# Kernel optimization log

Hardware: AMD Instinct MI355X
Metric: run time of the kernel (lower is better)

## Reference

```python
import jax, jax.numpy as jnp
import numpy as np

TOP_K = 2  # MoEBlock default


def setup_inputs() -> dict:
    key = jax.random.key(0)
    ks = jax.random.split(key, 7)
    B_, S, D, F, E, R = 2, 2048, 1024, 4096, 4, 4
    x  = jax.random.normal(ks[0], (B_, S, D), dtype=jnp.float32)
    Wg = jax.random.normal(ks[1], (E, D), dtype=jnp.float32) * (1.0 / np.sqrt(D))
    bg = jnp.zeros((E,), dtype=jnp.float32)
    Wi = jax.random.normal(ks[2], (F, D), dtype=jnp.float32) * (1.0 / np.sqrt(D))
    Wo = jax.random.normal(ks[3], (D, F), dtype=jnp.float32) * (1.0 / np.sqrt(F))
    A  = jax.random.normal(ks[4], (E, R, D), dtype=jnp.float32) * (1.0 / np.sqrt(D))
    Bm = jax.random.normal(ks[5], (E, F, R), dtype=jnp.float32) * 0.01
    return {"x": x, "Wg": Wg, "bg": bg, "Wi": Wi, "Wo": Wo, "A": A, "B": Bm}


def reference(x, Wg, bg, Wi, Wo, A, B):
    E = Wg.shape[0]
    # ---- Router: softmax gate + top-k ----
    logits = jnp.einsum('bsd,ed->bse', x, Wg) + bg          # [B,S,E]
    scores = jax.nn.softmax(logits, axis=-1)
    topv, topi = jax.lax.top_k(scores, TOP_K)               # [B,S,K]
    # per-token combine weight for each expert (sum of matching top-k probs)
    w = jnp.sum(jax.nn.one_hot(topi, E, dtype=x.dtype) * topv[..., None], axis=-2)  # [B,S,E]
    # ---- Experts: shared frozen FFN + per-expert LoRA (dense, then masked) ----
    base = jnp.einsum('bsd,fd->bsf', x, Wi)                 # shared wi(x), [B,S,F]
    lora_low = jnp.einsum('bsd,erd->bser', x, A)            # [B,S,E,R]
    lora = jnp.einsum('bser,efr->bsef', lora_low, B)        # [B,S,E,F]
    h = jax.nn.relu(base[:, :, None, :] + lora)             # act(wi(x)+lora), [B,S,E,F]
    expert_out = jnp.einsum('bsef,df->bsed', h, Wo)         # wo(.), [B,S,E,D]
    # ---- Combine ----
    out = jnp.einsum('bse,bsed->bsd', w, expert_out)        # [B,S,D]
    return out
```

## Files before the change

kernel.cpp:

```cpp
#include <hip/hip_runtime.h>
#include <stdint.h>

#define BSz 4096
#define Ddim 1024
#define Fdim 4096
#define Edim 4
#define Rdim 4

typedef __attribute__((ext_vector_type(8))) short bf16x8;
typedef __attribute__((ext_vector_type(4))) float f32x4;

__device__ __forceinline__ unsigned short f2bf(float f) {
  union { float f; uint32_t u; } c; c.f = f;
  return (unsigned short)((c.u + 0x7fffu + ((c.u >> 16) & 1u)) >> 16);
}

__global__ __launch_bounds__(256) void cvt2_kernel(const float* __restrict__ wi,
                                                   const float* __restrict__ wo,
                                                   unsigned short* __restrict__ wib,
                                                   unsigned short* __restrict__ wob,
                                                   int n4) {
  int i = blockIdx.x * 256 + threadIdx.x;
  if (i >= n4) return;
  const float* src = (blockIdx.y == 0) ? wi : wo;
  unsigned short* dst = (blockIdx.y == 0) ? wib : wob;
  float4 v = ((const float4*)src)[i];
  ushort4 o;
  o.x = f2bf(v.x); o.y = f2bf(v.y); o.z = f2bf(v.z); o.w = f2bf(v.w);
  ((ushort4*)dst)[i] = o;
}

__global__ __launch_bounds__(256) void router_cvtx(const float* __restrict__ x,
                                                   const float* __restrict__ Wg,
                                                   const float* __restrict__ bg,
                                                   const float* __restrict__ Aw,
                                                   unsigned short* __restrict__ xb,
                                                   float* __restrict__ meta) {
  __shared__ float xs[Ddim];
  __shared__ float dots[Edim + Edim * Rdim];
  const int t = blockIdx.x;
  const float4* xt = (const float4*)(x + (size_t)t * Ddim);
  {
    const int i = threadIdx.x;
    float4 v = xt[i];
    ((float4*)xs)[i] = v;
    ushort4 o;
    o.x = f2bf(v.x); o.y = f2bf(v.y); o.z = f2bf(v.z); o.w = f2bf(v.w);
    ((ushort4*)(xb + (size_t)t * Ddim))[i] = o;
  }
  __syncthreads();
  const int wave = threadIdx.x >> 6, lane = threadIdx.x & 63;
  for (int d = wave * 5; d < wave * 5 + 5; ++d) {
    const float* wrow = (d < Edim) ? (Wg + (size_t)d * Ddim)
                                   : (Aw + (size_t)(d - Edim) * Ddim);
    float s = 0.f;
    for (int i = lane; i < Ddim; i += 64) s += xs[i] * wrow[i];
    for (int off = 32; off; off >>= 1) s += __shfl_down(s, off);
    if (lane == 0) dots[d] = s;
  }
  __syncthreads();
  if (threadIdx.x == 0) {
    float p[Edim];
    float m = -1e30f;
    for (int e = 0; e < Edim; ++e) { p[e] = dots[e] + bg[e]; m = fmaxf(m, p[e]); }
    float sum = 0.f;
    for (int e = 0; e < Edim; ++e) { p[e] = expf(p[e] - m); sum += p[e]; }
    const float inv = 1.f / sum;
    for (int e = 0; e < Edim; ++e) p[e] *= inv;
    int e0 = 0;
    for (int e = 1; e < Edim; ++e) if (p[e] > p[e0]) e0 = e;
    int e1 = (e0 == 0) ? 1 : 0;
    for (int e = 0; e < Edim; ++e) if (e != e0 && p[e] > p[e1]) e1 = e;
    float* mt = meta + (size_t)t * 16;
    mt[0] = (float)e0; mt[1] = (float)e1; mt[2] = p[e0]; mt[3] = p[e1];
    for (int r = 0; r < Rdim; ++r) {
      mt[4 + r] = dots[Edim + e0 * Rdim + r];
      mt[8 + r] = dots[Edim + e1 * Rdim + r];
    }
    mt[12] = 0.f; mt[13] = 0.f; mt[14] = 0.f; mt[15] = 0.f;
  }
}

template <int EPI>
__global__ __launch_bounds__(256, 4)
void gemm97(const unsigned short* __restrict__ Ag,
            const unsigned short* __restrict__ Bg,
            int K, int kslice, int Ncols,
            const float* __restrict__ meta,
            const float* __restrict__ B2,
            unsigned short* __restrict__ outg,
            float* __restrict__ outf,
            float* __restrict__ zbuf) {
  constexpr int BK = 64;
  __shared__ __align__(16) unsigned short sA[128 * BK];
  __shared__ __align__(16) unsigned short sB[128 * BK];

  const int tid = threadIdx.x;
  const int lane = tid & 63;
  const int wave = tid >> 6;
  const int wr = wave >> 1, wc = wave & 1;
  const int l16 = lane & 15, lhi = lane >> 4;

  const int nwg = gridDim.x * gridDim.y;
  const int lin = blockIdx.y * gridDim.x + blockIdx.x;
  const int cpx = nwg >> 3;
  const int swz = (lin & 7) * cpx + (lin >> 3);
  const int bx = swz % gridDim.x, by = swz / gridDim.x;
  const int bm = by * 128, bn = bx * 128;
  const int kbase = blockIdx.z * kslice;
  const int NT = kslice / BK;

  if (EPI == 0) {
    const float4 z4 = make_float4(0.f, 0.f, 0.f, 0.f);
#pragma unroll
    for (int zz = 0; zz < 4; ++zz)
      ((float4*)zbuf)[(size_t)lin * 1024 + zz * 256 + tid] = z4;
  }

  f32x4 acc[4][4] = {};

  const int srow = tid >> 3;
  const int scol = ((tid & 7) ^ (srow & 7)) * 8;
  const int ldst = tid * 8;
  const int xr = l16 & 7;

  for (int kt = 0; kt < NT; ++kt) {
    const int kof = kbase + kt * BK;
#pragma unroll
    for (int rr = 0; rr < 4; ++rr)
      __builtin_amdgcn_global_load_lds(
          (const __attribute__((address_space(1))) void*)(Ag + (size_t)(bm + srow + rr * 32) * K + kof + scol),
          (__attribute__((address_space(3))) void*)(sA + ldst + rr * 2048), 16, 0, 0);
#pragma unroll
    for (int rr = 0; rr < 4; ++rr)
      __builtin_amdgcn_global_load_lds(
          (const __attribute__((address_space(1))) void*)(Bg + (size_t)(bn + srow + rr * 32) * K + kof + scol),
          (__attribute__((address_space(3))) void*)(sB + ldst + rr * 2048), 16, 0, 0);
    __syncthreads();
#pragma unroll
    for (int kk = 0; kk < 2; ++kk) {
      bf16x8 af[4], bfv[4];
#pragma unroll
      for (int i = 0; i < 4; ++i) {
        af[i] = *(const bf16x8*)(sA + (wr * 64 + i * 16 + l16) * BK + (((kk * 4 + lhi) ^ xr) * 8));
        bfv[i] = *(const bf16x8*)(sB + (wc * 64 + i * 16 + l16) * BK + (((kk * 4 + lhi) ^ xr) * 8));
      }
#pragma unroll
      for (int i = 0; i < 4; ++i)
#pragma unroll
        for (int j = 0; j < 4; ++j)
          acc[i][j] = __builtin_amdgcn_mfma_f32_16x16x32_bf16(af[i], bfv[j], acc[i][j], 0, 0, 0);
    }
    __syncthreads();
  }

  if (EPI == 0) {
#pragma unroll
    for (int mi = 0; mi < 4; ++mi) {
#pragma unroll
      for (int r = 0; r < 4; ++r) {
        const int rowl = wr * 64 + mi * 16 + lhi * 4 + r;
        const int row = bm + rowl;
        const float* mt = meta + (size_t)row * 16;
        const int e0 = (int)mt[0], e1 = (int)mt[1];
        const float w0 = mt[2], w1 = mt[3];
        const float4 l0 = *(const float4*)(mt + 4);
        const float4 l1 = *(const float4*)(mt + 8);
        unsigned short* trow = (rowl < 64 ? sA + rowl * 128 : sB + (rowl - 64) * 128);
#pragma unroll
        for (int ni = 0; ni < 4; ++ni) {
          const int coll = wc * 64 + ni * 16 + l16;
          const int f = bn + coll;
          const float4 b0 = *(const float4*)(B2 + ((size_t)e0 * Fdim + f) * Rdim);
          const float4 b1 = *(const float4*)(B2 + ((size_t)e1 * Fdim + f) * Rdim);
          const float a = acc[mi][ni][r];
          const float lora0 = l0.x * b0.x + l0.y * b0.y + l0.z * b0.z + l0.w * b0.w;
          const float lora1 = l1.x * b1.x + l1.y * b1.y + l1.z * b1.z + l1.w * b1.w;
          const float gv = w0 * fmaxf(a + lora0, 0.f) + w1 * fmaxf(a + lora1, 0.f);
          trow[coll] = f2bf(gv);
        }
      }
    }
    __syncthreads();
#pragma unroll
    for (int rnd = 0; rnd < 8; ++rnd) {
      const int idx = rnd * 256 + tid;
      const int rowl = idx >> 4;
      const int chk = idx & 15;
      const unsigned short* src = (rowl < 64 ? sA + rowl * 128 : sB + (rowl - 64) * 128) + chk * 8;
      *(bf16x8*)(outg + (size_t)(bm + rowl) * Fdim + bn + chk * 8) = *(const bf16x8*)src;
    }
  } else {
#pragma unroll
    for (int mi = 0; mi < 4; ++mi)
#pragma unroll
      for (int ni = 0; ni < 4; ++ni)
#pragma unroll
        for (int r = 0; r < 4; ++r) {
          const int row = bm + wr * 64 + mi * 16 + lhi * 4 + r;
          const int col = bn + wc * 64 + ni * 16 + l16;
          unsafeAtomicAdd(&outf[(size_t)row * Ncols + col], acc[mi][ni][r]);
        }
  }
}

extern "C" void kernel_launch(void* const* d_in, const int* in_sizes, int n_in,
                              void* d_out, int out_size, void* d_ws, size_t ws_size,
                              hipStream_t stream) {
  const float* x  = (const float*)d_in[0];
  const float* Wg = (const float*)d_in[1];
  const float* bg = (const float*)d_in[2];
  const float* Wi = (const float*)d_in[3];
  const float* Wo = (const float*)d_in[4];
  const float* Aw = (const float*)d_in[5];
  const float* B2 = (const float*)d_in[6];
  float* out = (float*)d_out;

  unsigned short* xb  = (unsigned short*)d_ws;
  unsigned short* wib = xb  + (size_t)BSz  * Ddim;
  unsigned short* wob = wib + (size_t)Fdim * Ddim;
  unsigned short* g   = wob + (size_t)Ddim * Fdim;
  float* meta = (float*)(g + (size_t)BSz * Fdim);

  const int n4 = Fdim * Ddim / 4;
  cvt2_kernel<<<dim3((n4 + 255) / 256, 2), 256, 0, stream>>>(
      Wi, Wo, wib, wob, n4);

  router_cvtx<<<BSz, 256, 0, stream>>>(x, Wg, bg, Aw, xb, meta);

  gemm97<0><<<dim3(Fdim / 128, BSz / 128, 1), 256, 0, stream>>>(
      xb, wib, Ddim, Ddim, Fdim, meta, B2, g, nullptr, out);

  gemm97<1><<<dim3(Ddim / 128, BSz / 128, 2), 256, 0, stream>>>(
      g, wob, Fdim, Fdim / 2, Ddim, nullptr, nullptr, nullptr, out, nullptr);
}
```

Measured before the change: 168.5 us.

## Fuse weight conversion into router kernel and enlarge first GEMM tile to 256x128

Merges the bf16 conversion of Wi/Wo into the router/x-conversion kernel as extra blocks, removing a separate launch and letting both run concurrently. The first GEMM gets a dedicated kernel with 512 threads and a 256x128 tile, increasing operand reuse per block and halving the grid in M. Its epilogue stages the output in two halves through shared memory. The larger block lowers per-CU occupancy and adds more sync steps in the epilogue.

```diff
diff --git a/kernel.cpp b/kernel.cpp
--- a/kernel.cpp
+++ b/kernel.cpp
@@ -15,34 +15,35 @@
   return (unsigned short)((c.u + 0x7fffu + ((c.u >> 16) & 1u)) >> 16);
 }
 
-__global__ __launch_bounds__(256) void cvt2_kernel(const float* __restrict__ wi,
-                                                   const float* __restrict__ wo,
-                                                   unsigned short* __restrict__ wib,
-                                                   unsigned short* __restrict__ wob,
-                                                   int n4) {
-  int i = blockIdx.x * 256 + threadIdx.x;
-  if (i >= n4) return;
-  const float* src = (blockIdx.y == 0) ? wi : wo;
-  unsigned short* dst = (blockIdx.y == 0) ? wib : wob;
-  float4 v = ((const float4*)src)[i];
-  ushort4 o;
-  o.x = f2bf(v.x); o.y = f2bf(v.y); o.z = f2bf(v.z); o.w = f2bf(v.w);
-  ((ushort4*)dst)[i] = o;
-}
-
-__global__ __launch_bounds__(256) void router_cvtx(const float* __restrict__ x,
+__global__ __launch_bounds__(256) void prep_kernel(const float* __restrict__ x,
                                                    const float* __restrict__ Wg,
                                                    const float* __restrict__ bg,
                                                    const float* __restrict__ Aw,
+                                                   const float* __restrict__ Wi,
+                                                   const float* __restrict__ Wo,
                                                    unsigned short* __restrict__ xb,
+                                                   unsigned short* __restrict__ wib,
+                                                   unsigned short* __restrict__ wob,
                                                    float* __restrict__ meta) {
+  const int b = blockIdx.x;
+  if (b >= BSz) {
+    const int n4 = Fdim * Ddim / 4;
+    int i = (b - BSz) * 256 + threadIdx.x;
+    const float* src = (i < n4) ? Wi : Wo;
+    unsigned short* dst = (i < n4) ? wib : wob;
+    if (i >= n4) i -= n4;
+    float4 v = ((const float4*)src)[i];
+    ushort4 o;
+    o.x = f2bf(v.x); o.y = f2bf(v.y); o.z = f2bf(v.z); o.w = f2bf(v.w);
+    ((ushort4*)dst)[i] = o;
+    return;
+  }
   __shared__ float xs[Ddim];
   __shared__ float dots[Edim + Edim * Rdim];
-  const int t = blockIdx.x;
-  const float4* xt = (const float4*)(x + (size_t)t * Ddim);
+  const int t = b;
   {
     const int i = threadIdx.x;
-    float4 v = xt[i];
+    float4 v = ((const float4*)(x + (size_t)t * Ddim))[i];
     ((float4*)xs)[i] = v;
     ushort4 o;
     o.x = f2bf(v.x); o.y = f2bf(v.y); o.z = f2bf(v.z); o.w = f2bf(v.w);
@@ -81,16 +82,121 @@
   }
 }
 
-template <int EPI>
+__global__ __launch_bounds__(512, 2)
+void gemm1_w(const unsigned short* __restrict__ Ag,
+             const unsigned short* __restrict__ Bg,
+             const float* __restrict__ meta,
+             const float* __restrict__ B2,
+             unsigned short* __restrict__ outg,
+             float* __restrict__ zbuf) {
+  constexpr int K = Ddim, BK = 64;
+  __shared__ __align__(16) unsigned short sA[256 * BK];
+  __shared__ __align__(16) unsigned short sB[128 * BK];
+
+  const int tid = threadIdx.x;
+  const int lane = tid & 63;
+  const int wave = tid >> 6;
+  const int wr = wave >> 1, wc = wave & 1;
+  const int l16 = lane & 15, lhi = lane >> 4;
+
+  const int nwg = gridDim.x * gridDim.y;
+  const int lin = blockIdx.y * gridDim.x + blockIdx.x;
+  const int cpx = nwg >> 3;
+  const int swz = (lin & 7) * cpx + (lin >> 3);
+  const int bx = swz % gridDim.x, by = swz / gridDim.x;
+  const int bm = by * 256, bn = bx * 128;
+
+  {
+    const float4 z4 = make_float4(0.f, 0.f, 0.f, 0.f);
+#pragma unroll
+    for (int zz = 0; zz < 4; ++zz)
+      ((float4*)zbuf)[(size_t)lin * 2048 + zz * 512 + tid] = z4;
+  }
+
+  f32x4 acc[4][4] = {};
+
+  const int srow = tid >> 3;
+  const int scol = ((tid & 7) ^ (srow & 7)) * 8;
+  const int ldst = tid * 8;
+  const int xr = l16 & 7;
+
+  for (int kt = 0; kt < K / BK; ++kt) {
+    const int kof = kt * BK;
+#pragma unroll
+    for (int rr = 0; rr < 4; ++rr)
+      __builtin_amdgcn_global_load_lds(
+          (const __attribute__((address_space(1))) void*)(Ag + (size_t)(bm + srow + rr * 64) * K + kof + scol),
+          (__attribute__((address_space(3))) void*)(sA + ldst + rr * 4096), 16, 0, 0);
+#pragma unroll
+    for (int rr = 0; rr < 2; ++rr)
+      __builtin_amdgcn_global_load_lds(
+          (const __attribute__((address_space(1))) void*)(Bg + (size_t)(bn + srow + rr * 64) * K + kof + scol),
+          (__attribute__((address_space(3))) void*)(sB + ldst + rr * 4096), 16, 0, 0);
+    __syncthreads();
+#pragma unroll
+    for (int kk = 0; kk < 2; ++kk) {
+      bf16x8 af[4], bfv[4];
+#pragma unroll
+      for (int i = 0; i < 4; ++i) {
+        af[i] = *(const bf16x8*)(sA + (wr * 64 + i * 16 + l16) * BK + (((kk * 4 + lhi) ^ xr) * 8));
+        bfv[i] = *(const bf16x8*)(sB + (wc * 64 + i * 16 + l16) * BK + (((kk * 4 + lhi) ^ xr) * 8));
+      }
+#pragma unroll
+      for (int i = 0; i < 4; ++i)
+#pragma unroll
+        for (int j = 0; j < 4; ++j)
+          acc[i][j] = __builtin_amdgcn_mfma_f32_16x16x32_bf16(af[i], bfv[j], acc[i][j], 0, 0, 0);
+    }
+    __syncthreads();
+  }
+
+#pragma unroll
+  for (int half = 0; half < 2; ++half) {
+    if ((wr >> 1) == half) {
+#pragma unroll
+      for (int mi = 0; mi < 4; ++mi) {
+#pragma unroll
+        for (int r = 0; r < 4; ++r) {
+          const int rowl = wr * 64 + mi * 16 + lhi * 4 + r;
+          const int row = bm + rowl;
+          const float* mt = meta + (size_t)row * 16;
+          const int e0 = (int)mt[0], e1 = (int)mt[1];
+          const float w0 = mt[2], w1 = mt[3];
+          const float4 l0 = *(const float4*)(mt + 4);
+          const float4 l1 = *(const float4*)(mt + 8);
+#pragma unroll
+          for (int ni = 0; ni < 4; ++ni) {
+            const int coll = wc * 64 + ni * 16 + l16;
+            const int f = bn + coll;
+            const float4 b0 = *(const float4*)(B2 + ((size_t)e0 * Fdim + f) * Rdim);
+            const float4 b1 = *(const float4*)(B2 + ((size_t)e1 * Fdim + f) * Rdim);
+            const float a = acc[mi][ni][r];
+            const float lora0 = l0.x * b0.x + l0.y * b0.y + l0.z * b0.z + l0.w * b0.w;
+            const float lora1 = l1.x * b1.x + l1.y * b1.y + l1.z * b1.z + l1.w * b1.w;
+            const float gv = w0 * fmaxf(a + lora0, 0.f) + w1 * fmaxf(a + lora1, 0.f);
+            sA[(rowl - half * 128) * 128 + coll] = f2bf(gv);
+          }
+        }
+      }
+    }
+    __syncthreads();
+#pragma unroll
+    for (int rnd = 0; rnd < 4; ++rnd) {
+      const int idx = rnd * 512 + tid;
+      const int rowl2 = idx >> 4;
+      const int chk = idx & 15;
+      *(bf16x8*)(outg + (size_t)(bm + half * 128 + rowl2) * Fdim + bn + chk * 8) =
+          *(const bf16x8*)(sA + rowl2 * 128 + chk * 8);
+    }
+    __syncthreads();
+  }
+}
+
 __global__ __launch_bounds__(256, 4)
-void gemm97(const unsigned short* __restrict__ Ag,
-            const unsigned short* __restrict__ Bg,
-            int K, int kslice, int Ncols,
-            const float* __restrict__ meta,
-            const float* __restrict__ B2,
-            unsigned short* __restrict__ outg,
-            float* __restrict__ outf,
-            float* __restrict__ zbuf) {
+void gemm2_w(const unsigned short* __restrict__ Ag,
+             const unsigned short* __restrict__ Bg,
+             int K, int kslice, int Ncols,
+             float* __restrict__ outf) {
   constexpr int BK = 64;
   __shared__ __align__(16) unsigned short sA[128 * BK];
   __shared__ __align__(16) unsigned short sB[128 * BK];
@@ -110,13 +216,6 @@
   const int kbase = blockIdx.z * kslice;
   const int NT = kslice / BK;
 
-  if (EPI == 0) {
-    const float4 z4 = make_float4(0.f, 0.f, 0.f, 0.f);
-#pragma unroll
-    for (int zz = 0; zz < 4; ++zz)
-      ((float4*)zbuf)[(size_t)lin * 1024 + zz * 256 + tid] = z4;
-  }
-
   f32x4 acc[4][4] = {};
 
   const int srow = tid >> 3;
@@ -154,54 +253,16 @@
     __syncthreads();
   }
 
-  if (EPI == 0) {
-#pragma unroll
-    for (int mi = 0; mi < 4; ++mi) {
+#pragma unroll
+  for (int mi = 0; mi < 4; ++mi)
+#pragma unroll
+    for (int ni = 0; ni < 4; ++ni)
 #pragma unroll
       for (int r = 0; r < 4; ++r) {
-        const int rowl = wr * 64 + mi * 16 + lhi * 4 + r;
-        const int row = bm + rowl;
-        const float* mt = meta + (size_t)row * 16;
-        const int e0 = (int)mt[0], e1 = (int)mt[1];
-        const float w0 = mt[2], w1 = mt[3];
-        const float4 l0 = *(const float4*)(mt + 4);
-        const float4 l1 = *(const float4*)(mt + 8);
-        unsigned short* trow = (rowl < 64 ? sA + rowl * 128 : sB + (rowl - 64) * 128);
-#pragma unroll
-        for (int ni = 0; ni < 4; ++ni) {
-          const int coll = wc * 64 + ni * 16 + l16;
-          const int f = bn + coll;
-          const float4 b0 = *(const float4*)(B2 + ((size_t)e0 * Fdim + f) * Rdim);
-          const float4 b1 = *(const float4*)(B2 + ((size_t)e1 * Fdim + f) * Rdim);
-          const float a = acc[mi][ni][r];
-          const float lora0 = l0.x * b0.x + l0.y * b0.y + l0.z * b0.z + l0.w * b0.w;
-          const float lora1 = l1.x * b1.x + l1.y * b1.y + l1.z * b1.z + l1.w * b1.w;
-          const float gv = w0 * fmaxf(a + lora0, 0.f) + w1 * fmaxf(a + lora1, 0.f);
-          trow[coll] = f2bf(gv);
-        }
-      }
-    }
-    __syncthreads();
-#pragma unroll
-    for (int rnd = 0; rnd < 8; ++rnd) {
-      const int idx = rnd * 256 + tid;
-      const int rowl = idx >> 4;
-      const int chk = idx & 15;
-      const unsigned short* src = (rowl < 64 ? sA + rowl * 128 : sB + (rowl - 64) * 128) + chk * 8;
-      *(bf16x8*)(outg + (size_t)(bm + rowl) * Fdim + bn + chk * 8) = *(const bf16x8*)src;
-    }
-  } else {
-#pragma unroll
-    for (int mi = 0; mi < 4; ++mi)
-#pragma unroll
-      for (int ni = 0; ni < 4; ++ni)
-#pragma unroll
-        for (int r = 0; r < 4; ++r) {
-          const int row = bm + wr * 64 + mi * 16 + lhi * 4 + r;
-          const int col = bn + wc * 64 + ni * 16 + l16;
-          unsafeAtomicAdd(&outf[(size_t)row * Ncols + col], acc[mi][ni][r]);
-        }
-  }
+        const int row = bm + wr * 64 + mi * 16 + lhi * 4 + r;
+        const int col = bn + wc * 64 + ni * 16 + l16;
+        unsafeAtomicAdd(&outf[(size_t)row * Ncols + col], acc[mi][ni][r]);
+      }
 }
 
 extern "C" void kernel_launch(void* const* d_in, const int* in_sizes, int n_in,
@@ -222,15 +283,12 @@
   unsigned short* g   = wob + (size_t)Ddim * Fdim;
   float* meta = (float*)(g + (size_t)BSz * Fdim);
 
-  const int n4 = Fdim * Ddim / 4;
-  cvt2_kernel<<<dim3((n4 + 255) / 256, 2), 256, 0, stream>>>(
-      Wi, Wo, wib, wob, n4);
-
-  router_cvtx<<<BSz, 256, 0, stream>>>(x, Wg, bg, Aw, xb, meta);
-
-  gemm97<0><<<dim3(Fdim / 128, BSz / 128, 1), 256, 0, stream>>>(
-      xb, wib, Ddim, Ddim, Fdim, meta, B2, g, nullptr, out);
-
-  gemm97<1><<<dim3(Ddim / 128, BSz / 128, 2), 256, 0, stream>>>(
-      g, wob, Fdim, Fdim / 2, Ddim, nullptr, nullptr, nullptr, out, nullptr);
-}
+  prep_kernel<<<BSz + 2 * (Fdim * Ddim / 4) / 256, 256, 0, stream>>>(
+      x, Wg, bg, Aw, Wi, Wo, xb, wib, wob, meta);
+
+  gemm1_w<<<dim3(Fdim / 128, BSz / 256), 512, 0, stream>>>(
+      xb, wib, meta, B2, g, out);
+
+  gemm2_w<<<dim3(Ddim / 128, BSz / 128, 2), 256, 0, stream>>>(
+      g, wob, Fdim, Fdim / 2, Ddim, out);
+}
```

Measured after the change: 184.0 us. 9.2% more time.
